# Kernel optimization log

Measured on AMD Instinct MI355X. Metric: run time of the kernel, lower is better.

Reference implementation:

```python
import jax, jax.numpy as jnp
import numpy as np
import itertools


def exclude_mask(n, d):
    # Boolean mask over d object axes of size n: True iff all indices pairwise distinct.
    if d <= 1:
        return jnp.ones((n,) * d, dtype=bool)
    idx = [jnp.arange(n).reshape((1,) * i + (n,) + (1,) * (d - 1 - i)) for i in range(d)]
    m = jnp.ones((n,) * d, dtype=bool)
    for i in range(d):
        for j in range(i + 1, d):
            m = m & (idx[i] != idx[j])
    return m


def reduce_group(x, d, exclude_self=True):
    # x: [B, n^d (d object axes), C] -> [B, n^(d-1), 2C]
    # exists = max over last object axis (masked to 0), forall = min (masked to 1),
    # interleaved per channel as in torch.stack(..., dim=-1).view(..., 2C).
    if exclude_self and d > 1:
        n = x.shape[1]
        m = exclude_mask(n, d)[None, ..., None]
        x0 = jnp.where(m, x, 0.0)
        x1 = jnp.where(m, x, 1.0)
    else:
        x0 = x1 = x
    ex = jnp.max(x0, axis=-2)
    fa = jnp.min(x1, axis=-2)
    out = jnp.stack([ex, fa], axis=-1)  # [..., C, 2]
    return out.reshape(out.shape[:-2] + (out.shape[-2] * 2,))


def expand_group(x, n):
    # Insert a new object axis of size n just before the channel axis (broadcast).
    return jnp.broadcast_to(jnp.expand_dims(x, -2), x.shape[:-1] + (n, x.shape[-1]))


def permute_group(x, d):
    # Concatenate all d! permutations of the last d object axes along channels.
    if d <= 1:
        return x
    nd = x.ndim
    obj_axes = list(range(nd - 1 - d, nd - 1))
    res = []
    for perm in itertools.permutations(obj_axes):
        p = list(range(0, nd - 1 - d)) + list(perm) + [nd - 1]
        res.append(jnp.transpose(x, p))
    return jnp.concatenate(res, axis=-1)


def mlp(x, W1, b1, W2, b2):
    # InferenceLayer: Linear -> ReLU -> Linear -> Sigmoid, applied on channel dim.
    h = jax.nn.relu(x @ W1 + b1)
    return jax.nn.sigmoid(h @ W2 + b2)


def setup_inputs() -> dict:
    key = jax.random.key(0)
    ks = jax.random.split(key, 24)
    B, n, C, H = 4, 48, 16, 64
    cin = {0: 48, 1: 64, 2: 128, 3: 192}
    inp = {
        "x0": jax.random.uniform(ks[0], (B, C), dtype=jnp.float32),
        "x1": jax.random.uniform(ks[1], (B, n, C), dtype=jnp.float32),
        "x2": jax.random.uniform(ks[2], (B, n, n, C), dtype=jnp.float32),
        "x3": jax.random.uniform(ks[3], (B, n, n, n, C), dtype=jnp.float32),
    }
    for g in range(4):
        inp[f"W1_{g}"] = 0.05 * jax.random.normal(ks[4 + 4 * g], (cin[g], H), dtype=jnp.float32)
        inp[f"b1_{g}"] = jnp.zeros((H,), dtype=jnp.float32)
        inp[f"W2_{g}"] = 0.05 * jax.random.normal(ks[5 + 4 * g], (H, C), dtype=jnp.float32)
        inp[f"b2_{g}"] = jnp.zeros((C,), dtype=jnp.float32)
    return inp


def reference(x0, x1, x2, x3,
              W1_0, b1_0, W2_0, b2_0,
              W1_1, b1_1, W2_1, b2_1,
              W1_2, b1_2, W2_2, b2_2,
              W1_3, b1_3, W2_3, b2_3):
    n = x1.shape[1]
    # group 0: [self, reduce(group1)] -> MLP
    t0 = jnp.concatenate([x0, reduce_group(x1, 1)], axis=-1)            # [B, 48]
    o0 = mlp(t0, W1_0, b1_0, W2_0, b2_0)
    # group 1: [expand(group0), self, reduce(group2)] -> MLP (permuter d=1 is identity)
    t1 = jnp.concatenate([expand_group(x0, n), x1, reduce_group(x2, 2)], axis=-1)  # [B,n,64]
    o1 = mlp(t1, W1_1, b1_1, W2_1, b2_1)
    # group 2: [expand(group1), self, reduce(group3)] -> permute(d=2) -> MLP
    t2 = jnp.concatenate([expand_group(x1, n), x2, reduce_group(x3, 3)], axis=-1)  # [B,n,n,64]
    t2 = permute_group(t2, 2)                                           # [B,n,n,128]
    o2 = mlp(t2, W1_2, b1_2, W2_2, b2_2)
    # group 3: [expand(group2), self] -> permute(d=3) -> MLP
    t3 = jnp.concatenate([expand_group(x2, n), x3], axis=-1)            # [B,n,n,n,32]
    t3 = permute_group(t3, 3)                                           # [B,n,n,n,192]
    o3 = mlp(t3, W1_3, b1_3, W2_3, b2_3)
    return (o0, o1, o2, o3)
```

## Files before the change

kernel.cpp:

```cpp
#include <hip/hip_runtime.h>
#include <hip/hip_bf16.h>
#include <math.h>

#define NN 48

typedef __attribute__((ext_vector_type(8))) short bf16x8;
typedef __attribute__((ext_vector_type(4))) float f32x4;

__device__ __forceinline__ float sigmoidf_(float x) {
    return 1.0f / (1.0f + __expf(-x));
}

__device__ __forceinline__ unsigned short f2bf(float f) {
    __hip_bfloat16 h = __float2bfloat16(f);
    unsigned short u;
    __builtin_memcpy(&u, &h, 2);
    return u;
}

__device__ __forceinline__ unsigned packbf2(float a, float b) {
    return (unsigned)f2bf(a) | ((unsigned)f2bf(b) << 16);
}

__global__ __launch_bounds__(256) void k_pre(const float* __restrict__ x2, const float* __restrict__ x3,
        const float* __restrict__ W1, const float* __restrict__ W2,
        float* __restrict__ r3, unsigned short* __restrict__ wf,
        unsigned short* __restrict__ x2bf, unsigned short* __restrict__ x3bf, int emit) {
    int tid = threadIdx.x, blk = blockIdx.x;
    if (blk < 2304) {
        int posl = tid >> 6, l = tid & 63;
        int pos = blk * 4 + posl;
        int j = pos % NN, i = (pos / NN) % NN;
        int cq = l & 3, kkb = l >> 2;
        float4 ex = make_float4(0.f, 0.f, 0.f, 0.f);
        float4 fa = make_float4(1.f, 1.f, 1.f, 1.f);
        #pragma unroll
        for (int s = 0; s < 3; ++s) {
            int kk = kkb + s * 16;
            size_t idx = (((size_t)pos * NN + kk) << 4) + (cq << 2);
            float4 v = *(const float4*)(x3 + idx);
            if (emit) {
                uint2 pk;
                pk.x = packbf2(v.x, v.y);
                pk.y = packbf2(v.z, v.w);
                *(uint2*)(x3bf + idx) = pk;
            }
            bool ok = (i != j) && (kk != i) && (kk != j);
            ex.x = fmaxf(ex.x, ok ? v.x : 0.f);  fa.x = fminf(fa.x, ok ? v.x : 1.f);
            ex.y = fmaxf(ex.y, ok ? v.y : 0.f);  fa.y = fminf(fa.y, ok ? v.y : 1.f);
            ex.z = fmaxf(ex.z, ok ? v.z : 0.f);  fa.z = fminf(fa.z, ok ? v.z : 1.f);
            ex.w = fmaxf(ex.w, ok ? v.w : 0.f);  fa.w = fminf(fa.w, ok ? v.w : 1.f);
        }
        #pragma unroll
        for (int m = 4; m <= 32; m <<= 1) {
            ex.x = fmaxf(ex.x, __shfl_xor(ex.x, m));  fa.x = fminf(fa.x, __shfl_xor(fa.x, m));
            ex.y = fmaxf(ex.y, __shfl_xor(ex.y, m));  fa.y = fminf(fa.y, __shfl_xor(fa.y, m));
            ex.z = fmaxf(ex.z, __shfl_xor(ex.z, m));  fa.z = fminf(fa.z, __shfl_xor(fa.z, m));
            ex.w = fmaxf(ex.w, __shfl_xor(ex.w, m));  fa.w = fminf(fa.w, __shfl_xor(fa.w, m));
        }
        if (kkb == 0) {
            float* dst = r3 + ((size_t)pos << 5) + (cq << 3);
            *(float4*)dst       = make_float4(ex.x, fa.x, ex.y, fa.y);
            *(float4*)(dst + 4) = make_float4(ex.z, fa.z, ex.w, fa.w);
        }
    } else if (blk < 2340) {
        if (!emit) return;
        int bb = blk - 2304;
        #pragma unroll
        for (int q = 0; q < 4; ++q) {
            int e = bb * 1024 + q * 256 + tid;
            int off = e << 2;
            float4 v = *(const float4*)(x2 + off);
            uint2 pk;
            pk.x = packbf2(v.x, v.y);
            pk.y = packbf2(v.z, v.w);
            *(uint2*)(x2bf + off) = pk;
        }
    } else {
        for (int e = tid; e < 13312; e += 256) {
            unsigned short v;
            if (e < 12288) {
                int idx = e & 7, l = (e >> 3) & 63, r = e >> 9;
                int ks = r % 6, nt = r / 6;
                v = f2bf(W1[(ks * 32 + ((l >> 4) << 3) + idx) * 64 + (nt << 4) + (l & 15)]);
            } else {
                int e2 = e - 12288;
                int idx = e2 & 7, l = (e2 >> 3) & 63, ks = e2 >> 9;
                v = f2bf(W2[(ks * 32 + ((l >> 4) << 3) + idx) * 16 + (l & 15)]);
            }
            wf[e] = v;
        }
    }
}

__global__ __launch_bounds__(256) void k_small(const float* __restrict__ x0, const float* __restrict__ x1,
        const float* __restrict__ x2, const float* __restrict__ r3,
        const float* __restrict__ W1_0, const float* __restrict__ b1_0,
        const float* __restrict__ W2_0, const float* __restrict__ b2_0,
        const float* __restrict__ W1_1, const float* __restrict__ b1_1,
        const float* __restrict__ W2_1, const float* __restrict__ b2_1,
        const float* __restrict__ W1_2, const float* __restrict__ b1_2,
        const float* __restrict__ W2_2, const float* __restrict__ b2_2,
        float* __restrict__ out) {
    __shared__ __align__(16) float smem[8960];
    int tid = threadIdx.x;
    int blk = blockIdx.x;
    if (blk == 0) {
        float* st0 = smem;
        float* sh0 = smem + 192;
        int b = tid >> 6, sub = (tid >> 4) & 3, c = tid & 15;
        float ex = -INFINITY, fa = INFINITY;
        for (int ii = sub * 12; ii < sub * 12 + 12; ++ii) {
            float v = x1[(b * NN + ii) * 16 + c];
            ex = fmaxf(ex, v); fa = fminf(fa, v);
        }
        ex = fmaxf(ex, __shfl_xor(ex, 16)); fa = fminf(fa, __shfl_xor(fa, 16));
        ex = fmaxf(ex, __shfl_xor(ex, 32)); fa = fminf(fa, __shfl_xor(fa, 32));
        if (sub == 0) { st0[b * 48 + 16 + 2 * c] = ex; st0[b * 48 + 17 + 2 * c] = fa; }
        if (tid < 64) st0[(tid >> 4) * 48 + (tid & 15)] = x0[tid];
        __syncthreads();
        {
            int bb = tid >> 6, ln = tid & 63;
            float h = b1_0[ln];
            for (int cc = 0; cc < 48; ++cc) h += st0[bb * 48 + cc] * W1_0[cc * 64 + ln];
            sh0[bb * 64 + ln] = fmaxf(h, 0.f);
        }
        __syncthreads();
        if (tid < 64) {
            int bb = tid >> 4, o = tid & 15;
            float acc = b2_0[o];
            for (int tt = 0; tt < 64; ++tt) acc += sh0[bb * 64 + tt] * W2_0[tt * 16 + o];
            out[bb * 16 + o] = sigmoidf_(acc);
        }
    } else if (blk <= 48) {
        int grp = tid >> 6, ln = tid & 63;
        int row = (blk - 1) * 4 + grp;
        int b = row / NN, i = row % NN;
        float* sin1 = smem + grp * 64;
        float* sh1  = smem + 256 + grp * 64;
        int c = ln & 15, q = ln >> 4;
        float ex = 0.f, fa = 1.f;
        const float* xb = x2 + (size_t)row * NN * 16 + c;
        for (int jj = q * 12; jj < q * 12 + 12; ++jj) {
            float v = xb[jj * 16];
            bool ok = (jj != i);
            ex = fmaxf(ex, ok ? v : 0.f); fa = fminf(fa, ok ? v : 1.f);
        }
        ex = fmaxf(ex, __shfl_xor(ex, 16)); fa = fminf(fa, __shfl_xor(fa, 16));
        ex = fmaxf(ex, __shfl_xor(ex, 32)); fa = fminf(fa, __shfl_xor(fa, 32));
        if (q == 0) { sin1[32 + 2 * c] = ex; sin1[33 + 2 * c] = fa; }
        if (ln < 16) sin1[ln] = x0[b * 16 + ln];
        else if (ln < 32) sin1[ln] = x1[row * 16 + (ln - 16)];
        __syncthreads();
        float h = b1_1[ln];
        #pragma unroll
        for (int c4 = 0; c4 < 64; c4 += 4) {
            float4 iv = *(const float4*)&sin1[c4];
            h += iv.x * W1_1[(c4 + 0) * 64 + ln] + iv.y * W1_1[(c4 + 1) * 64 + ln]
               + iv.z * W1_1[(c4 + 2) * 64 + ln] + iv.w * W1_1[(c4 + 3) * 64 + ln];
        }
        sh1[ln] = fmaxf(h, 0.f);
        __syncthreads();
        if (ln < 16) {
            float acc = b2_1[ln];
            #pragma unroll
            for (int tt = 0; tt < 64; ++tt) acc += sh1[tt] * W2_1[tt * 16 + ln];
            out[64 + row * 16 + ln] = sigmoidf_(acc);
        }
    } else {
        float* sW1  = smem;
        float* sin_ = smem + 8192;
        float* sh   = smem + 8704;
        int wv = tid >> 6, ln = tid & 63;
        for (int p = tid; p < 8192; p += 256) sW1[p] = W1_2[p];
        float bias = b1_2[ln];
        __syncthreads();
        for (int rr = 0; rr < 4; ++rr) {
            int row = (blk - 49) * 16 + rr * 4 + wv;
            int j = row % NN;
            int bi = row / NN;
            int i = bi % NN;
            int b = bi / NN;
            for (int cc = ln; cc < 128; cc += 64) {
                int half = cc >> 6, w = cc & 63;
                int a1 = half ? j : i;
                int a2 = half ? i : j;
                float v;
                if (w < 16)      v = x1[(b * NN + a1) * 16 + w];
                else if (w < 32) v = x2[((b * NN + a1) * NN + a2) * 16 + (w - 16)];
                else             v = r3[((size_t)(b * NN + a1) * NN + a2) * 32 + (w - 32)];
                sin_[wv * 128 + cc] = v;
            }
            __syncthreads();
            float h = bias;
            #pragma unroll
            for (int c4 = 0; c4 < 128; c4 += 4) {
                float4 iv = *(const float4*)&sin_[wv * 128 + c4];
                h += iv.x * sW1[(c4 + 0) * 64 + ln] + iv.y * sW1[(c4 + 1) * 64 + ln]
                   + iv.z * sW1[(c4 + 2) * 64 + ln] + iv.w * sW1[(c4 + 3) * 64 + ln];
            }
            sh[wv * 64 + ln] = fmaxf(h, 0.f);
            __syncthreads();
            if (ln < 16) {
                float acc = b2_2[ln];
                #pragma unroll
                for (int tt = 0; tt < 64; ++tt) acc += sh[wv * 64 + tt] * W2_2[tt * 16 + ln];
                out[3136 + row * 16 + ln] = sigmoidf_(acc);
            }
            __syncthreads();
        }
    }
}

__global__ __launch_bounds__(192) void k_g3d(const unsigned short* __restrict__ x2bf,
        const unsigned short* __restrict__ x3bf, const unsigned short* __restrict__ wf,
        const float* __restrict__ b1, const float* __restrict__ b2,
        float* __restrict__ out3) {
    __shared__ __align__(16) unsigned short sH[2][6 * 64 * 8];

    int tid = threadIdx.x, mt = tid >> 6, l = tid & 63;
    int pp = blockIdx.x, i = 0;
    while (pp >= NN - i) { pp -= NN - i; ++i; }
    int j = i + pp;
    int b = blockIdx.y;

    bf16x8 w1f[4][6];
    #pragma unroll
    for (int nt = 0; nt < 4; ++nt)
        #pragma unroll
        for (int ks = 0; ks < 6; ++ks)
            w1f[nt][ks] = *(const bf16x8*)(wf + (((nt * 6 + ks) << 6) + l) * 8);
    bf16x8 w2f[2];
    #pragma unroll
    for (int ks = 0; ks < 2; ++ks)
        w2f[ks] = *(const bf16x8*)(wf + 12288 + ((ks << 6) + l) * 8);

    const int b2b = b * 36864;
    const int b3b = b * 1769472;
    const int cb2_[6] = { b2b + (i * NN + j) * 16, b2b + i * 768, b2b + (j * NN + i) * 16,
                          b2b + i * 16,            b2b + j * 768, b2b + j * 16 };
    const int cb3_[6] = { b3b + (i * NN + j) * 768, b3b + i * 36864 + j * 16, b3b + (j * NN + i) * 768,
                          b3b + i * 768 + j * 16,   b3b + j * 36864 + i * 16, b3b + j * 768 + i * 16 };
    const int s2_[6] = { 0, 16, 0, 768, 16, 768 };
    const int s3_[6] = { 16, 768, 16, 36864, 768, 36864 };

    int l15 = l & 15, g = l >> 4;
    bool isx2 = (g < 2);
    int goff = (g & 1) << 3;
    const unsigned short* bp = isx2 ? x2bf : x3bf;
    int off_[6];
    #pragma unroll
    for (int f = 0; f < 6; ++f) {
        int s = isx2 ? s2_[f] : s3_[f];
        int base = isx2 ? cb2_[f] : cb3_[f];
        off_[f] = base + ((mt << 4) + l15) * s + goff;
    }

    f32x4 acc[4][2];
    #pragma unroll
    for (int nt = 0; nt < 4; ++nt) {
        float bv = b1[(nt << 4) + l15];
        f32x4 t = {bv, bv, bv, bv};
        acc[nt][0] = t; acc[nt][1] = t;
    }
    const int p1[6] = { 2, 4, 0, 5, 1, 3 };

    #pragma unroll
    for (int f = 0; f < 6; ++f) {
        bf16x8 a = *(const bf16x8*)(bp + off_[f]);
        #pragma unroll
        for (int nt = 0; nt < 4; ++nt) {
            acc[nt][0] = __builtin_amdgcn_mfma_f32_16x16x32_bf16(a, w1f[nt][f], acc[nt][0], 0, 0, 0);
            acc[nt][1] = __builtin_amdgcn_mfma_f32_16x16x32_bf16(a, w1f[nt][p1[f]], acc[nt][1], 0, 0, 0);
        }
    }

    {
        int rbase = (l >> 4) << 2;
        #pragma unroll
        for (int tr = 0; tr < 2; ++tr) {
            #pragma unroll
            for (int nt = 0; nt < 4; ++nt) {
                int within = ((nt & 1) << 4) + l15;
                int ks2 = nt >> 1;
                int lhi = (within >> 3) << 4;
                int idx = within & 7;
                #pragma unroll
                for (int rg = 0; rg < 4; ++rg) {
                    float h = fmaxf(acc[nt][tr][rg], 0.0f);
                    int lp = rbase + rg + lhi;
                    sH[tr][((((mt << 1) + ks2) << 6) + lp) * 8 + idx] = f2bf(h);
                }
            }
        }
    }
    __syncthreads();

    {
        float bv2 = b2[l15];
        #pragma unroll
        for (int tr = 0; tr < 2; ++tr) {
            if (tr == 0 || i != j) {
                f32x4 acc2 = {bv2, bv2, bv2, bv2};
                #pragma unroll
                for (int ks = 0; ks < 2; ++ks) {
                    bf16x8 a = *(const bf16x8*)&sH[tr][((((mt << 1) + ks) << 6) + l) << 3];
                    acc2 = __builtin_amdgcn_mfma_f32_16x16x32_bf16(a, w2f[ks], acc2, 0, 0, 0);
                }
                int triple = tr ? ((b * NN + j) * NN + i) : ((b * NN + i) * NN + j);
                size_t obase = ((size_t)triple * NN + (mt << 4) + ((l >> 4) << 2)) * 16 + l15;
                #pragma unroll
                for (int rg = 0; rg < 4; ++rg)
                    out3[obase + (size_t)rg * 16] = sigmoidf_(acc2[rg]);
            }
        }
    }
}

__global__ __launch_bounds__(256) void k_g3m(const float* __restrict__ x2, const float* __restrict__ x3,
                                             const unsigned short* __restrict__ wf,
                                             const float* __restrict__ b1, const float* __restrict__ b2,
                                             float* __restrict__ out3) {
    __shared__ __align__(16) unsigned short sA[18 * 64 * 8];
    __shared__ __align__(16) unsigned short sH[6 * 64 * 8];

    int tid = threadIdx.x;
    int wv = tid >> 6, l = tid & 63;
    int triple = blockIdx.x;
    int j = triple % NN;
    int bi = triple / NN;
    int i = bi % NN;
    int b = bi / NN;

    bf16x8 w1f[6];
    #pragma unroll
    for (int ks = 0; ks < 6; ++ks)
        w1f[ks] = *(const bf16x8*)(wf + (((wv * 6 + ks) << 6) + l) * 8);
    bf16x8 w2f[2];
    #pragma unroll
    for (int ks = 0; ks < 2; ++ks)
        w2f[ks] = *(const bf16x8*)(wf + 12288 + ((ks << 6) + l) * 8);

    const int x2b = b * NN * NN * 16;
    const int x3b = b * NN * NN * NN * 16;

    #pragma unroll
    for (int it = 0; it < 9; ++it) {
        int t = it * 256 + tid;
        int fs = __builtin_amdgcn_readfirstlane(t >> 7);
        int mt = fs / 6;
        int ks = fs - mt * 6;
        int lp = (t >> 1) & 63;
        int kk = (mt << 4) + (lp & 15);
        int w = ((lp >> 4) << 3) + ((t & 1) << 2);
        int a1, a2, a3;
        switch (ks) {
            case 0:  a1 = i;  a2 = j;  a3 = kk; break;
            case 1:  a1 = i;  a2 = kk; a3 = j;  break;
            case 2:  a1 = j;  a2 = i;  a3 = kk; break;
            case 3:  a1 = kk; a2 = i;  a3 = j;  break;
            case 4:  a1 = j;  a2 = kk; a3 = i;  break;
            default: a1 = kk; a2 = j;  a3 = i;  break;
        }
        const float* p2 = x2 + x2b + (a1 * NN + a2) * 16 + w;
        const float* p3 = x3 + x3b + ((a1 * NN + a2) * NN + a3) * 16 + (w - 16);
        const float* p = (w < 16) ? p2 : p3;
        float4 v = *(const float4*)p;
        uint2 pk;
        pk.x = packbf2(v.x, v.y);
        pk.y = packbf2(v.z, v.w);
        *(uint2*)&sA[t * 4] = pk;
    }
    __syncthreads();

    float bv = b1[(wv << 4) + (l & 15)];
    f32x4 acc0 = {bv, bv, bv, bv};
    f32x4 acc1 = acc0, acc2 = acc0;
    #pragma unroll
    for (int ks = 0; ks < 6; ++ks) {
        bf16x8 a0  = *(const bf16x8*)&sA[(((0 * 6 + ks) << 6) + l) << 3];
        bf16x8 a1_ = *(const bf16x8*)&sA[(((1 * 6 + ks) << 6) + l) << 3];
        bf16x8 a2_ = *(const bf16x8*)&sA[(((2 * 6 + ks) << 6) + l) << 3];
        acc0 = __builtin_amdgcn_mfma_f32_16x16x32_bf16(a0,  w1f[ks], acc0, 0, 0, 0);
        acc1 = __builtin_amdgcn_mfma_f32_16x16x32_bf16(a1_, w1f[ks], acc1, 0, 0, 0);
        acc2 = __builtin_amdgcn_mfma_f32_16x16x32_bf16(a2_, w1f[ks], acc2, 0, 0, 0);
    }

    {
        int within = ((wv & 1) << 4) + (l & 15);
        int ks2 = wv >> 1;
        int lhi = (within >> 3) << 4;
        int idx = within & 7;
        int rbase = (l >> 4) << 2;
        #pragma unroll
        for (int mt = 0; mt < 3; ++mt) {
            f32x4 a = (mt == 0) ? acc0 : (mt == 1) ? acc1 : acc2;
            #pragma unroll
            for (int rg = 0; rg < 4; ++rg) {
                float h = fmaxf(a[rg], 0.0f);
                int lp = rbase + rg + lhi;
                sH[((((mt << 1) + ks2) << 6) + lp) * 8 + idx] = f2bf(h);
            }
        }
    }
    __syncthreads();

    if (wv < 3) {
        int mt = wv;
        float bv2 = b2[l & 15];
        f32x4 acc = {bv2, bv2, bv2, bv2};
        #pragma unroll
        for (int ks = 0; ks < 2; ++ks) {
            bf16x8 a = *(const bf16x8*)&sH[((((mt << 1) + ks) << 6) + l) << 3];
            acc = __builtin_amdgcn_mfma_f32_16x16x32_bf16(a, w2f[ks], acc, 0, 0, 0);
        }
        size_t obase = ((size_t)triple * NN + (mt << 4) + ((l >> 4) << 2)) * 16 + (l & 15);
        #pragma unroll
        for (int rg = 0; rg < 4; ++rg)
            out3[obase + (size_t)rg * 16] = sigmoidf_(acc[rg]);
    }
}

extern "C" void kernel_launch(void* const* d_in, const int* in_sizes, int n_in,
                              void* d_out, int out_size, void* d_ws, size_t ws_size,
                              hipStream_t stream) {
    const float* x0 = (const float*)d_in[0];
    const float* x1 = (const float*)d_in[1];
    const float* x2 = (const float*)d_in[2];
    const float* x3 = (const float*)d_in[3];
    const float* W1_0 = (const float*)d_in[4];
    const float* b1_0 = (const float*)d_in[5];
    const float* W2_0 = (const float*)d_in[6];
    const float* b2_0 = (const float*)d_in[7];
    const float* W1_1 = (const float*)d_in[8];
    const float* b1_1 = (const float*)d_in[9];
    const float* W2_1 = (const float*)d_in[10];
    const float* b2_1 = (const float*)d_in[11];
    const float* W1_2 = (const float*)d_in[12];
    const float* b1_2 = (const float*)d_in[13];
    const float* W2_2 = (const float*)d_in[14];
    const float* b2_2 = (const float*)d_in[15];
    const float* W1_3 = (const float*)d_in[16];
    const float* b1_3 = (const float*)d_in[17];
    const float* W2_3 = (const float*)d_in[18];
    const float* b2_3 = (const float*)d_in[19];

    float* out = (float*)d_out;
    float* r3 = (float*)d_ws;
    unsigned short* wf   = (unsigned short*)(r3 + 294912);
    unsigned short* x2bf = wf + 13312;
    unsigned short* x3bf = x2bf + 147456;
    size_t need = (size_t)294912 * 4 + (size_t)(13312 + 147456 + 7077888) * 2;
    int fast = (ws_size >= need) ? 1 : 0;

    hipLaunchKernelGGL(k_pre, dim3(2341), dim3(256), 0, stream,
                       x2, x3, W1_3, W2_3, r3, wf, x2bf, x3bf, fast);
    if (fast)
        hipLaunchKernelGGL(k_g3d, dim3(1176, 4), dim3(192), 0, stream,
                           x2bf, x3bf, wf, b1_3, b2_3, out + 150592);
    else
        hipLaunchKernelGGL(k_g3m, dim3(9216), dim3(256), 0, stream,
                           x2, x3, wf, b1_3, b2_3, out + 150592);
    hipLaunchKernelGGL(k_small, dim3(625), dim3(256), 0, stream,
                       x0, x1, x2, r3,
                       W1_0, b1_0, W2_0, b2_0,
                       W1_1, b1_1, W2_1, b2_1,
                       W1_2, b1_2, W2_2, b2_2,
                       out);
}
```

Measured before the change: 80.34 us.

## Precompute transposed bf16 copies of x2/x3 so group-3 gathers are contiguous

The preprocessing kernel now writes two extra permuted bf16 copies of x3 (zbf, ybf) and a transposed bf16 copy of x2 (x2t) into an enlarged workspace. The group-3 MFMA kernel indexes all six permutation operands from one base pointer, and every lane now reads consecutive rows at a 16-element stride instead of the large 768 or 36864 strides. The aim is to remove uncoalesced, cache-unfriendly gathers in the main kernel. In exchange, the preprocessing kernel writes roughly twice as much extra data, and its scatter stores to the transposed layouts are poorly coalesced. The block barrier between the hidden-layer LDS write and the second MFMA read is also dropped, relying on each wave reading only its own LDS slice.

```diff
diff --git a/kernel.cpp b/kernel.cpp
--- a/kernel.cpp
+++ b/kernel.cpp
@@ -25,12 +25,17 @@
 __global__ __launch_bounds__(256) void k_pre(const float* __restrict__ x2, const float* __restrict__ x3,
         const float* __restrict__ W1, const float* __restrict__ W2,
         float* __restrict__ r3, unsigned short* __restrict__ wf,
-        unsigned short* __restrict__ x2bf, unsigned short* __restrict__ x3bf, int emit) {
+        unsigned short* __restrict__ x2bf, unsigned short* __restrict__ x2t,
+        unsigned short* __restrict__ x3bf, unsigned short* __restrict__ zbf,
+        unsigned short* __restrict__ ybf, int emit) {
     int tid = threadIdx.x, blk = blockIdx.x;
     if (blk < 2304) {
         int posl = tid >> 6, l = tid & 63;
         int pos = blk * 4 + posl;
-        int j = pos % NN, i = (pos / NN) % NN;
+        int j = pos % NN;
+        int bi = pos / NN;
+        int i = bi % NN;
+        int b = bi / NN;
         int cq = l & 3, kkb = l >> 2;
         float4 ex = make_float4(0.f, 0.f, 0.f, 0.f);
         float4 fa = make_float4(1.f, 1.f, 1.f, 1.f);
@@ -44,6 +49,10 @@
                 pk.x = packbf2(v.x, v.y);
                 pk.y = packbf2(v.z, v.w);
                 *(uint2*)(x3bf + idx) = pk;
+                size_t zi = ((size_t)bi * NN + kk) * 768 + j * 16 + (cq << 2);
+                *(uint2*)(zbf + zi) = pk;
+                size_t yi = ((size_t)(b * NN + j) * NN + kk) * 768 + i * 16 + (cq << 2);
+                *(uint2*)(ybf + yi) = pk;
             }
             bool ok = (i != j) && (kk != i) && (kk != j);
             ex.x = fmaxf(ex.x, ok ? v.x : 0.f);  fa.x = fminf(fa.x, ok ? v.x : 1.f);
@@ -67,14 +76,22 @@
         if (!emit) return;
         int bb = blk - 2304;
         #pragma unroll
-        for (int q = 0; q < 4; ++q) {
-            int e = bb * 1024 + q * 256 + tid;
+        for (int q4 = 0; q4 < 4; ++q4) {
+            int e = bb * 1024 + q4 * 256 + tid;
             int off = e << 2;
             float4 v = *(const float4*)(x2 + off);
             uint2 pk;
             pk.x = packbf2(v.x, v.y);
             pk.y = packbf2(v.z, v.w);
             *(uint2*)(x2bf + off) = pk;
+            int c = off & 15;
+            int r = off >> 4;
+            int q = r % NN;
+            int bp = r / NN;
+            int p = bp % NN;
+            int b_ = bp / NN;
+            int ti = (((b_ * NN + q) * NN + p) << 4) + c;
+            *(uint2*)(x2t + ti) = pk;
         }
     } else {
         for (int e = tid; e < 13312; e += 256) {
@@ -212,8 +229,8 @@
     }
 }
 
-__global__ __launch_bounds__(192) void k_g3d(const unsigned short* __restrict__ x2bf,
-        const unsigned short* __restrict__ x3bf, const unsigned short* __restrict__ wf,
+__global__ __launch_bounds__(192) void k_g3d(const unsigned short* __restrict__ wsb,
+        const unsigned short* __restrict__ wf,
         const float* __restrict__ b1, const float* __restrict__ b2,
         float* __restrict__ out3) {
     __shared__ __align__(16) unsigned short sH[2][6 * 64 * 8];
@@ -237,23 +254,30 @@
 
     const int b2b = b * 36864;
     const int b3b = b * 1769472;
-    const int cb2_[6] = { b2b + (i * NN + j) * 16, b2b + i * 768, b2b + (j * NN + i) * 16,
-                          b2b + i * 16,            b2b + j * 768, b2b + j * 16 };
-    const int cb3_[6] = { b3b + (i * NN + j) * 768, b3b + i * 36864 + j * 16, b3b + (j * NN + i) * 768,
-                          b3b + i * 768 + j * 16,   b3b + j * 36864 + i * 16, b3b + j * 768 + i * 16 };
-    const int s2_[6] = { 0, 16, 0, 768, 16, 768 };
-    const int s3_[6] = { 16, 768, 16, 36864, 768, 36864 };
+    const int p1[6] = { 2, 4, 0, 5, 1, 3 };
 
     int l15 = l & 15, g = l >> 4;
     bool isx2 = (g < 2);
     int goff = (g & 1) << 3;
-    const unsigned short* bp = isx2 ? x2bf : x3bf;
+    int ij16 = (i * NN + j) * 16, ji16 = (j * NN + i) * 16;
+    int row16 = ((mt << 4) + l15) << 4;
+
     int off_[6];
-    #pragma unroll
-    for (int f = 0; f < 6; ++f) {
-        int s = isx2 ? s2_[f] : s3_[f];
-        int base = isx2 ? cb2_[f] : cb3_[f];
-        off_[f] = base + ((mt << 4) + l15) * s + goff;
+    if (isx2) {
+        off_[0] = b2b + ij16 + goff;
+        off_[1] = b2b + i * 768 + row16 + goff;
+        off_[2] = b2b + ji16 + goff;
+        off_[3] = 147456 + b2b + i * 768 + row16 + goff;
+        off_[4] = b2b + j * 768 + row16 + goff;
+        off_[5] = 147456 + b2b + j * 768 + row16 + goff;
+    } else {
+        int ij768 = (i * NN + j) * 768, ji768 = (j * NN + i) * 768;
+        off_[0] = 294912   + b3b + ij768 + row16 + goff;
+        off_[1] = 7372800  + b3b + ij768 + row16 + goff;
+        off_[2] = 294912   + b3b + ji768 + row16 + goff;
+        off_[3] = 14450688 + b3b + ij768 + row16 + goff;
+        off_[4] = 7372800  + b3b + ji768 + row16 + goff;
+        off_[5] = 14450688 + b3b + ji768 + row16 + goff;
     }
 
     f32x4 acc[4][2];
@@ -263,11 +287,10 @@
         f32x4 t = {bv, bv, bv, bv};
         acc[nt][0] = t; acc[nt][1] = t;
     }
-    const int p1[6] = { 2, 4, 0, 5, 1, 3 };
 
     #pragma unroll
     for (int f = 0; f < 6; ++f) {
-        bf16x8 a = *(const bf16x8*)(bp + off_[f]);
+        bf16x8 a = *(const bf16x8*)(wsb + off_[f]);
         #pragma unroll
         for (int nt = 0; nt < 4; ++nt) {
             acc[nt][0] = __builtin_amdgcn_mfma_f32_16x16x32_bf16(a, w1f[nt][f], acc[nt][0], 0, 0, 0);
@@ -294,7 +317,6 @@
             }
         }
     }
-    __syncthreads();
 
     {
         float bv2 = b2[l15];
@@ -449,15 +471,19 @@
     float* r3 = (float*)d_ws;
     unsigned short* wf   = (unsigned short*)(r3 + 294912);
     unsigned short* x2bf = wf + 13312;
-    unsigned short* x3bf = x2bf + 147456;
-    size_t need = (size_t)294912 * 4 + (size_t)(13312 + 147456 + 7077888) * 2;
+    unsigned short* x2t  = x2bf + 147456;
+    unsigned short* x3bf = x2t + 147456;
+    unsigned short* zbf  = x3bf + 7077888;
+    unsigned short* ybf  = zbf + 7077888;
+    size_t need = (size_t)294912 * 4
+                + (size_t)(13312 + 2 * 147456 + 3 * 7077888) * 2;
     int fast = (ws_size >= need) ? 1 : 0;
 
     hipLaunchKernelGGL(k_pre, dim3(2341), dim3(256), 0, stream,
-                       x2, x3, W1_3, W2_3, r3, wf, x2bf, x3bf, fast);
+                       x2, x3, W1_3, W2_3, r3, wf, x2bf, x2t, x3bf, zbf, ybf, fast);
     if (fast)
         hipLaunchKernelGGL(k_g3d, dim3(1176, 4), dim3(192), 0, stream,
-                           x2bf, x3bf, wf, b1_3, b2_3, out + 150592);
+                           x2bf, wf, b1_3, b2_3, out + 150592);
     else
         hipLaunchKernelGGL(k_g3m, dim3(9216), dim3(256), 0, stream,
                            x2, x3, wf, b1_3, b2_3, out + 150592);
```

New measurement: 78.59 us (median of 2 runs). 2.2% less time.
